# Optimization experiments

Measured on AMD Instinct MI355X. Metric: run time of the kernel, lower is better.

Reference implementation:

```python
import jax, jax.numpy as jnp
import numpy as np

N_WIRES = 12
N_QLAYERS = 2
DIM = 2 ** N_WIRES


def setup_inputs() -> dict:
    key = jax.random.key(0)
    k0, k1, k2, k3 = jax.random.split(key, 4)
    x = jax.random.normal(k0, (2048, 1024), dtype=jnp.float32)
    # TT cores: ranks [1,16,1], input dims [32,32], output dims [8,9]
    core0 = jax.random.normal(k1, (1, 32, 8, 16), dtype=jnp.float32) * 0.05
    core1 = jax.random.normal(k2, (16, 32, 9, 1), dtype=jnp.float32) * 0.05
    tt_bias = jnp.zeros((72,), dtype=jnp.float32)
    global_angles = jax.random.normal(k3, (N_QLAYERS, N_WIRES, 3), dtype=jnp.float32) * 0.1
    return {"x": x, "core0": core0, "core1": core1, "tt_bias": tt_bias,
            "global_angles": global_angles}


def _rot(angles):
    # angles [..., 3] -> combined U = Rz @ Ry @ Rx, shape [..., 2, 2] complex64
    half = angles * 0.5
    cx, sx = jnp.cos(half[..., 0]), jnp.sin(half[..., 0])
    cy, sy = jnp.cos(half[..., 1]), jnp.sin(half[..., 1])
    cz, sz = jnp.cos(half[..., 2]), jnp.sin(half[..., 2])
    zero = jnp.zeros_like(cx)
    cplx = jax.lax.complex
    Rx = jnp.stack([jnp.stack([cplx(cx, zero), cplx(zero, -sx)], -1),
                    jnp.stack([cplx(zero, -sx), cplx(cx, zero)], -1)], -2)
    Ry = jnp.stack([jnp.stack([cplx(cy, zero), cplx(-sy, zero)], -1),
                    jnp.stack([cplx(sy, zero), cplx(cy, zero)], -1)], -2)
    ez, ezc = cplx(cz, -sz), cplx(cz, sz)  # exp(-i z/2), exp(+i z/2)
    zc = cplx(zero, zero)
    Rz = jnp.stack([jnp.stack([ez, zc], -1), jnp.stack([zc, ezc], -1)], -2)
    return jnp.einsum('...ij,...jk,...kl->...il', Rz, Ry, Rx)


def _apply_1q(state, U, w):
    # state [bsz, 2^n]; U [bsz, 2, 2]; wire 0 = most significant qubit
    bsz = state.shape[0]
    left, right = 2 ** w, 2 ** (N_WIRES - w - 1)
    s = state.reshape(bsz, left, 2, right)
    s = jnp.einsum('bij,bljr->blir', U, s)
    return s.reshape(bsz, DIM)


def _cnot(state, c, t):
    bsz = state.shape[0]
    s = state.reshape((bsz,) + (2,) * N_WIRES)
    s0 = jax.lax.index_in_dim(s, 0, c + 1, keepdims=True)
    s1 = jax.lax.index_in_dim(s, 1, c + 1, keepdims=True)
    s1 = jnp.flip(s1, axis=t + 1)  # flip target amplitudes where control = 1
    return jnp.concatenate([s0, s1], axis=c + 1).reshape(bsz, DIM)


def reference(x, core0, core1, tt_bias, global_angles):
    bsz = x.shape[0]
    # --- TT layer: x[b,32,32] contracted with two TT cores -> [b,8,9] -> [b,72]
    x_rs = x.reshape(bsz, 32, 32)
    tt_out = jnp.einsum('bij,aipq,qjrs->bpr', x_rs, core0, core1).reshape(bsz, -1) + tt_bias
    # residual global angles
    angles = global_angles[None, :, :, :] + tt_out.reshape(bsz, N_QLAYERS, N_WIRES, 3)
    U = _rot(angles)  # [bsz, L, n, 2, 2]
    # --- tensor-product Ry encoding of x[:, :n_wires] on |0...0>
    enc = x[:, :N_WIRES] * 0.5
    amp = jnp.stack([jnp.cos(enc), jnp.sin(enc)], -1)  # [bsz, n, 2]
    state = amp[:, 0, :]
    for w in range(1, N_WIRES):
        state = (state[:, :, None] * amp[:, w, None, :]).reshape(bsz, -1)
    state = state.astype(jnp.complex64)  # [bsz, 2^n]
    # --- VQC layers: fused Rz@Ry@Rx per wire, then ring CNOT (noise_prob=0)
    for k in range(N_QLAYERS):
        for w in range(N_WIRES):
            state = _apply_1q(state, U[:, k, w], w)
        for i in range(N_WIRES - 1):
            state = _cnot(state, i, i + 1)
        state = _cnot(state, N_WIRES - 1, 0)
    # --- MeasureAll(PauliZ): <Z_w> per wire
    probs = jnp.real(state * jnp.conj(state))  # [bsz, 2^n]
    idx = jnp.arange(DIM)[:, None]
    bits = (idx >> jnp.arange(N_WIRES - 1, -1, -1)[None, :]) & 1  # [2^n, n]
    zsign = (1.0 - 2.0 * bits).astype(jnp.float32)
    return probs @ zsign  # [bsz, n_wires]
```

## Files before the change

kernel.cpp:

```cpp
#include <hip/hip_runtime.h>
#include <math.h>

#define N_WIRES 12

__host__ __device__ constexpr int parity12(int x) {
  x ^= x >> 8; x ^= x >> 4; x ^= x >> 2; x ^= x >> 1;
  return x & 1;
}

__global__ __launch_bounds__(256) void build_w_kernel(
    const float* __restrict__ core0,
    const float* __restrict__ core1,
    float* __restrict__ Wt) {
  int idx = blockIdx.x * 256 + threadIdx.x;
  int k = idx / 72;
  int o = idx - k * 72;
  int i = k >> 5, jj = k & 31;
  int p = o / 9, r = o - p * 9;
  float acc = 0.f;
#pragma unroll
  for (int q = 0; q < 16; ++q) {
    acc += core0[(i * 8 + p) * 16 + q] * core1[(q * 32 + jj) * 9 + r];
  }
  int og = o / 9, j = o - og * 9;
  Wt[k * 96 + og * 12 + j] = acc;
}

__global__ __launch_bounds__(512) void tt_gemm2(
    const float* __restrict__ x,
    const float* __restrict__ Wt,
    const float* __restrict__ bias,
    float* __restrict__ ttout) {
  __shared__ __align__(16) float ws[128 * 96];
  __shared__ __align__(16) float xs[8 * 132];
  __shared__ float part[16 * 8 * 73];
  const int t = threadIdx.x;
  const int row0 = blockIdx.x * 8;
  const int kk = t >> 5;
  const int rp = (t >> 3) & 3;
  const int og = t & 7;
  const int r0 = rp * 2;

  float a0[9], a1[9];
#pragma unroll
  for (int j = 0; j < 9; ++j) { a0[j] = 0.f; a1[j] = 0.f; }

  for (int s = 0; s < 8; ++s) {
    __syncthreads();
    const float4* Wg = (const float4*)(Wt + s * 128 * 96);
#pragma unroll
    for (int i = 0; i < 6; ++i) {
      const int idx = i * 512 + t;
      ((float4*)ws)[idx] = Wg[idx];
    }
    if (t < 256) {
      const int rr = t >> 5, j4 = t & 31;
      *(float4*)&xs[rr * 132 + j4 * 4] =
          *(const float4*)(x + (size_t)(row0 + rr) * 1024 + s * 128 + j4 * 4);
    }
    __syncthreads();
#pragma unroll
    for (int i = 0; i < 8; ++i) {
      const int k = kk + i * 16;
      const float4 wA = *(const float4*)&ws[k * 96 + og * 12];
      const float4 wB = *(const float4*)&ws[k * 96 + og * 12 + 4];
      const float w8 = ws[k * 96 + og * 12 + 8];
      const float x0v = xs[r0 * 132 + k];
      const float x1v = xs[r0 * 132 + 132 + k];
      a0[0] += x0v * wA.x; a0[1] += x0v * wA.y;
      a0[2] += x0v * wA.z; a0[3] += x0v * wA.w;
      a0[4] += x0v * wB.x; a0[5] += x0v * wB.y;
      a0[6] += x0v * wB.z; a0[7] += x0v * wB.w;
      a0[8] += x0v * w8;
      a1[0] += x1v * wA.x; a1[1] += x1v * wA.y;
      a1[2] += x1v * wA.z; a1[3] += x1v * wA.w;
      a1[4] += x1v * wB.x; a1[5] += x1v * wB.y;
      a1[6] += x1v * wB.z; a1[7] += x1v * wB.w;
      a1[8] += x1v * w8;
    }
  }

#pragma unroll
  for (int j = 0; j < 9; ++j) {
    part[(kk * 8 + r0) * 73 + og * 9 + j] = a0[j];
    part[(kk * 8 + r0 + 1) * 73 + og * 9 + j] = a1[j];
  }
  __syncthreads();

  for (int i = t; i < 576; i += 512) {
    const int r = i / 72, o = i - r * 72;
    float ssum = bias[o];
#pragma unroll
    for (int kq = 0; kq < 16; ++kq) ssum += part[(kq * 8 + r) * 73 + o];
    ttout[(size_t)(row0 + r) * 72 + o] = ssum;
  }
}

template <int MASK, int ROW>
__device__ __forceinline__ void apply_gate(
    float vr[16], float vi[16],
    float u00r, float u00i, float u01r, float u01i,
    float u10r, float u10i, float u11r, float u11i,
    float* __restrict__ buf, int t) {
  constexpr int RM = MASK & 15;
  constexpr int TM = (MASK >> 4) & 0xFF;
  constexpr int LM = TM & 63;
  constexpr bool LDSX = (TM & 0xC0) != 0;

  const int tpar = __popc(ROW & (t << 4)) & 1;
  const float aor = tpar ? u11r : u00r, aoi = tpar ? u11i : u00i;
  const float apr = tpar ? u10r : u01r, api = tpar ? u10i : u01i;
  const float qor = tpar ? u00r : u11r, qoi = tpar ? u00i : u11i;
  const float qpr = tpar ? u01r : u10r, qpi = tpar ? u01i : u10i;

  auto upd = [&](int r, float ar, float ai, float br, float bi,
                 float& xr, float& xi) {
    const bool b1 = parity12(ROW & r);
    const float cor = b1 ? qor : aor, coi = b1 ? qoi : aoi;
    const float cpr = b1 ? qpr : apr, cpi = b1 ? qpi : api;
    const float nr = cor * ar - coi * ai + cpr * br - cpi * bi;
    const float ni = cor * ai + coi * ar + cpr * bi + cpi * br;
    xr = nr; xi = ni;
  };

  if constexpr (LDSX) {
    const int tp = t ^ TM;
    if constexpr ((RM & 8) == 0) {
      __syncthreads();
#pragma unroll
      for (int r = 8; r < 16; ++r) {
        buf[(r & 7) * 256 + t] = vr[r];
        buf[2048 + (r & 7) * 256 + t] = vi[r];
      }
      __syncthreads();
#pragma unroll
      for (int r = 8; r < 16; ++r) {
        const int r2 = r ^ RM;
        const float br = buf[(r2 & 7) * 256 + tp];
        const float bi = buf[2048 + (r2 & 7) * 256 + tp];
        upd(r, vr[r], vi[r], br, bi, vr[r], vi[r]);
      }
      __syncthreads();
#pragma unroll
      for (int r = 0; r < 8; ++r) {
        buf[r * 256 + t] = vr[r];
        buf[2048 + r * 256 + t] = vi[r];
      }
      __syncthreads();
#pragma unroll
      for (int r = 0; r < 8; ++r) {
        const int r2 = r ^ RM;
        const float br = buf[r2 * 256 + tp];
        const float bi = buf[2048 + r2 * 256 + tp];
        upd(r, vr[r], vi[r], br, bi, vr[r], vi[r]);
      }
    } else {
      __syncthreads();
#pragma unroll
      for (int r = 8; r < 16; ++r) {
        buf[(r & 7) * 256 + t] = vr[r];
        buf[2048 + (r & 7) * 256 + t] = vi[r];
      }
      __syncthreads();
      float tr[8], ti[8];
#pragma unroll
      for (int r = 0; r < 8; ++r) {
        const int r2 = r ^ RM;
        const float br = buf[(r2 & 7) * 256 + tp];
        const float bi = buf[2048 + (r2 & 7) * 256 + tp];
        upd(r, vr[r], vi[r], br, bi, tr[r], ti[r]);
      }
      __syncthreads();
#pragma unroll
      for (int r = 0; r < 8; ++r) {
        buf[r * 256 + t] = vr[r];
        buf[2048 + r * 256 + t] = vi[r];
      }
      __syncthreads();
#pragma unroll
      for (int r = 8; r < 16; ++r) {
        const int r2 = r ^ RM;
        const float br = buf[r2 * 256 + tp];
        const float bi = buf[2048 + r2 * 256 + tp];
        upd(r, vr[r], vi[r], br, bi, vr[r], vi[r]);
      }
#pragma unroll
      for (int r = 0; r < 8; ++r) { vr[r] = tr[r]; vi[r] = ti[r]; }
    }
  } else if constexpr (LM != 0) {
    static_assert(!(LM != 0) || RM == 0, "shfl gates have no reg component");
#pragma unroll
    for (int r = 0; r < 16; ++r) {
      const float br = __shfl_xor(vr[r], LM, 64);
      const float bi = __shfl_xor(vi[r], LM, 64);
      upd(r, vr[r], vi[r], br, bi, vr[r], vi[r]);
    }
  } else {
#pragma unroll
    for (int r = 0; r < 16; ++r) {
      if (r < (r ^ RM)) {
        const int r2 = r ^ RM;
        const float ar = vr[r], ai = vi[r];
        const float br = vr[r2], bi = vi[r2];
        upd(r, ar, ai, br, bi, vr[r], vi[r]);
        upd(r2, br, bi, ar, ai, vr[r2], vi[r2]);
      }
    }
  }
}

__global__ __launch_bounds__(256, 5) void vqc_kernel3(
    const float* __restrict__ x,
    const float* __restrict__ ttout,
    const float* __restrict__ gang,
    float* __restrict__ out) {
  const int b = blockIdx.x;
  const int t = threadIdx.x;

  __shared__ __align__(16) float buf[4096];
  __shared__ float sUre[12][4], sUim[12][4];
  __shared__ float sFre[12][2], sFim[12][2];

  const float* ttb = ttout + (size_t)b * 72;

  if (t < 24) {
    const int w = (t < 12) ? t : t - 12;
    const int k = (t < 12) ? 1 : 0;
    const int gbase = (k * 12 + w) * 3;
    const int tbase = k * 36 + w * 3;
    float a0 = gang[gbase + 0] + ttb[tbase + 0];
    float a1 = gang[gbase + 1] + ttb[tbase + 1];
    float a2 = gang[gbase + 2] + ttb[tbase + 2];
    float cx = cosf(0.5f * a0), sx = sinf(0.5f * a0);
    float cy = cosf(0.5f * a1), sy = sinf(0.5f * a1);
    float cz = cosf(0.5f * a2), sz = sinf(0.5f * a2);
    float m00r = cy * cx,   m00i = sy * sx;
    float m01r = -sy * cx,  m01i = -cy * sx;
    float m10r = sy * cx,   m10i = -cy * sx;
    float m11r = cy * cx,   m11i = -sy * sx;
    float U00r = cz * m00r + sz * m00i, U00i = cz * m00i - sz * m00r;
    float U01r = cz * m01r + sz * m01i, U01i = cz * m01i - sz * m01r;
    float U10r = cz * m10r - sz * m10i, U10i = cz * m10i + sz * m10r;
    float U11r = cz * m11r - sz * m11i, U11i = cz * m11i + sz * m11r;
    if (t < 12) {
      sUre[w][0] = U00r; sUim[w][0] = U00i;
      sUre[w][1] = U01r; sUim[w][1] = U01i;
      sUre[w][2] = U10r; sUim[w][2] = U10i;
      sUre[w][3] = U11r; sUim[w][3] = U11i;
    } else {
      const float e = x[(size_t)b * 1024 + w] * 0.5f;
      const float c = cosf(e), s = sinf(e);
      sFre[w][0] = U00r * c + U01r * s;  sFim[w][0] = U00i * c + U01i * s;
      sFre[w][1] = U10r * c + U11r * s;  sFim[w][1] = U10i * c + U11i * s;
    }
  }
  __syncthreads();

  float vr[16], vi[16];
  {
    const int bits[7] = {(t >> 7) & 1,
                         ((t >> 6) ^ (t >> 5)) & 1,
                         ((t >> 5) ^ (t >> 4)) & 1,
                         ((t >> 4) ^ (t >> 3)) & 1,
                         ((t >> 3) ^ (t >> 2)) & 1,
                         ((t >> 2) ^ (t >> 1)) & 1,
                         ((t >> 1) ^ t) & 1};
    float br_ = 1.f, bi_ = 0.f;
#pragma unroll
    for (int w = 0; w < 7; ++w) {
      const float fr = sFre[w][bits[w]], fi = sFim[w][bits[w]];
      const float nr = br_ * fr - bi_ * fi;
      const float ni = br_ * fi + bi_ * fr;
      br_ = nr; bi_ = ni;
    }
    const int t0 = t & 1;
    float b7r[2], b7i[2];
#pragma unroll
    for (int r3 = 0; r3 < 2; ++r3) {
      const float fr = sFre[7][t0 ^ r3], fi = sFim[7][t0 ^ r3];
      b7r[r3] = br_ * fr - bi_ * fi;
      b7i[r3] = br_ * fi + bi_ * fr;
    }
    float hr[8], hi[8];
#pragma unroll
    for (int j = 0; j < 8; ++j) {
      const int r3 = j >> 2, r2 = (j >> 1) & 1, r1 = j & 1;
      const float ar = sFre[8][r3 ^ r2], ai = sFim[8][r3 ^ r2];
      const float cr = sFre[9][r2 ^ r1], ci = sFim[9][r2 ^ r1];
      hr[j] = ar * cr - ai * ci; hi[j] = ar * ci + ai * cr;
    }
    float gr[4], gi[4];
#pragma unroll
    for (int j = 0; j < 4; ++j) {
      const int r1 = j >> 1, r0 = j & 1;
      const float ar = sFre[10][r1 ^ r0], ai = sFim[10][r1 ^ r0];
      const float cr = sFre[11][r0], ci = sFim[11][r0];
      gr[j] = ar * cr - ai * ci; gi[j] = ar * ci + ai * cr;
    }
#pragma unroll
    for (int r = 0; r < 16; ++r) {
      const int r3 = r >> 3, hj = r >> 1, gj = r & 3;
      const float pr = hr[hj] * gr[gj] - hi[hj] * gi[gj];
      const float pi = hr[hj] * gi[gj] + hi[hj] * gr[gj];
      vr[r] = b7r[r3] * pr - b7i[r3] * pi;
      vi[r] = b7r[r3] * pi + b7i[r3] * pr;
    }
  }

#define GATE(MASK, ROW, GID)                                             \
  apply_gate<MASK, ROW>(vr, vi,                                          \
      sUre[GID][0], sUim[GID][0], sUre[GID][1], sUim[GID][1],            \
      sUre[GID][2], sUim[GID][2], sUre[GID][3], sUim[GID][3], buf, t)

  GATE(0xC00, 0x400, 0);
  GATE(0x200, 0xE00, 1);
  GATE(0x100, 0xD00, 2);
  GATE(0x080, 0xC80, 3);
  GATE(0x040, 0xC40, 4);
  GATE(0x020, 0xC20, 5);
  GATE(0x010, 0xC10, 6);
  GATE(0x008, 0xC08, 7);
  GATE(0x004, 0xC04, 8);
  GATE(0x002, 0xC02, 9);
  GATE(0x001, 0xC01, 10);
  GATE(0xBFF, 0xC00, 11);
#undef GATE

  constexpr int MROWS[12] = {0xFFF, 0xA00, 0x700, 0xB80, 0x7C0, 0xBE0,
                             0x7F0, 0xBF8, 0x7FC, 0xBFE, 0x7FF, 0xBFF};
  float acc[12];
#pragma unroll
  for (int w = 0; w < 12; ++w) acc[w] = 0.f;
#pragma unroll
  for (int r = 0; r < 16; ++r) {
    const float pr = vr[r] * vr[r] + vi[r] * vi[r];
#pragma unroll
    for (int w = 0; w < 12; ++w) {
      if (parity12(MROWS[w] & r)) acc[w] -= pr; else acc[w] += pr;
    }
  }
  __syncthreads();
#pragma unroll
  for (int w = 0; w < 12; ++w) {
    float v = (__popc(MROWS[w] & (t << 4)) & 1) ? -acc[w] : acc[w];
#pragma unroll
    for (int off = 32; off > 0; off >>= 1) v += __shfl_down(v, off, 64);
    if ((t & 63) == 0) buf[(t >> 6) * 12 + w] = v;
  }
  __syncthreads();
  if (t < 12) {
    out[(size_t)b * 12 + t] = buf[t] + buf[12 + t] + buf[24 + t] + buf[36 + t];
  }
}

extern "C" void kernel_launch(void* const* d_in, const int* in_sizes, int n_in,
                              void* d_out, int out_size, void* d_ws, size_t ws_size,
                              hipStream_t stream) {
  const float* x       = (const float*)d_in[0];
  const float* core0   = (const float*)d_in[1];
  const float* core1   = (const float*)d_in[2];
  const float* tt_bias = (const float*)d_in[3];
  const float* gang    = (const float*)d_in[4];
  float* out = (float*)d_out;
  float* Wt     = (float*)d_ws;
  float* ttout  = (float*)d_ws + 98304;

  const int bsz = in_sizes[0] / 1024;

  build_w_kernel<<<288, 256, 0, stream>>>(core0, core1, Wt);
  tt_gemm2<<<bsz / 8, 512, 0, stream>>>(x, Wt, tt_bias, ttout);
  vqc_kernel3<<<bsz, 256, 0, stream>>>(x, ttout, gang, out);
}
```

Before: 58.89 us.

## Pack statevector amplitudes into float2 pairs and use packed FMA gate updates

Reorganizes the per-thread statevector into float2 pairs of amplitudes whose gate coefficients are related by sign, so each gate update runs through v_pk_fma_f32/v_pk_mul_f32 inline asm. It exploits the SU(2) structure of the gate matrix (only u00 and u01 are needed) and turns the per-thread parity into sign-bit XORs. The LDS exchange is rewritten into two phases using float2 stores. The goal is to cut VALU instruction count in the gate-heavy loop, at the cost of swap moves, inline-asm register constraints, and more complex indexing.

After: 58.79 us. No clear change (-0.2%).

```diff
diff --git a/kernel.cpp b/kernel.cpp
--- a/kernel.cpp
+++ b/kernel.cpp
@@ -7,6 +7,19 @@
   x ^= x >> 8; x ^= x >> 4; x ^= x >> 2; x ^= x >> 1;
   return x & 1;
 }
+
+typedef float2 f2;
+__device__ __forceinline__ f2 mk2(float a, float b) { f2 r; r.x = a; r.y = b; return r; }
+__device__ __forceinline__ f2 pkmul(f2 a, f2 b) {
+  f2 d; asm("v_pk_mul_f32 %0, %1, %2" : "=v"(d) : "v"(a), "v"(b)); return d;
+}
+__device__ __forceinline__ f2 pkfma(f2 a, f2 b, f2 c) {
+  f2 d; asm("v_pk_fma_f32 %0, %1, %2, %3" : "=v"(d) : "v"(a), "v"(b), "v"(c)); return d;
+}
+__device__ __forceinline__ f2 shfl_xor2(f2 v, int m) {
+  f2 r; r.x = __shfl_xor(v.x, m, 64); r.y = __shfl_xor(v.y, m, 64); return r;
+}
+__device__ __forceinline__ f2 swap2(f2 v) { return mk2(v.y, v.x); }
 
 __global__ __launch_bounds__(256) void build_w_kernel(
     const float* __restrict__ core0,
@@ -97,119 +110,93 @@
 }
 
 template <int MASK, int ROW>
-__device__ __forceinline__ void apply_gate(
-    float vr[16], float vi[16],
+__device__ __forceinline__ void gate_pk(f2 R[8], f2 I[8],
     float u00r, float u00i, float u01r, float u01i,
-    float u10r, float u10i, float u11r, float u11i,
-    float* __restrict__ buf, int t) {
+    f2* __restrict__ buf, int t) {
   constexpr int RM = MASK & 15;
   constexpr int TM = (MASK >> 4) & 0xFF;
   constexpr int LM = TM & 63;
   constexpr bool LDSX = (TM & 0xC0) != 0;
-
-  const int tpar = __popc(ROW & (t << 4)) & 1;
-  const float aor = tpar ? u11r : u00r, aoi = tpar ? u11i : u00i;
-  const float apr = tpar ? u10r : u01r, api = tpar ? u10i : u01i;
-  const float qor = tpar ? u00r : u11r, qoi = tpar ? u00i : u11i;
-  const float qpr = tpar ? u01r : u10r, qpi = tpar ? u01i : u10i;
-
-  auto upd = [&](int r, float ar, float ai, float br, float bi,
-                 float& xr, float& xi) {
-    const bool b1 = parity12(ROW & r);
-    const float cor = b1 ? qor : aor, coi = b1 ? qoi : aoi;
-    const float cpr = b1 ? qpr : apr, cpi = b1 ? qpi : api;
-    const float nr = cor * ar - coi * ai + cpr * br - cpi * bi;
-    const float ni = cor * ai + coi * ar + cpr * bi + cpi * br;
-    xr = nr; xi = ni;
+  constexpr int FLIP = parity12(ROW & 3);
+  constexpr int JX = (RM == 0) ? 0 : (((RM & 1) ? (RM ^ 3) : RM) >> 1);
+  constexpr bool SW = (RM & 1) != 0;
+
+  const int tsgn = (__popc(ROW & (t << 4)) & 1) << 31;
+  const float dEi = __int_as_float(__float_as_int(u00i) ^ tsgn);
+  const float oEr = __int_as_float(__float_as_int(u01r) ^ tsgn);
+  const float ndEi = -dEi, noEr = -oEr;
+  const f2 A  = mk2(u00r, u00r);
+  const f2 C  = mk2(u01i, u01i);
+  const f2 nC = mk2(-u01i, -u01i);
+
+  auto Dof = [&](int pe, int ph) { return mk2(pe ? ndEi : dEi, ph ? ndEi : dEi); };
+  auto Oof = [&](int pe, int ph) { return mk2(pe ? noEr : oEr, ph ? noEr : oEr); };
+
+  auto upd = [&](int j, f2 Rb, f2 Ib, f2& outR, f2& outI) {
+    const int pe = parity12(ROW & (2 * j));
+    const int ph = pe ^ FLIP;
+    const f2 Dj = Dof(pe, ph), nDj = Dof(!pe, !ph), Oj = Oof(pe, ph);
+    const f2 a = R[j], ii = I[j];
+    outR = pkfma(A, a, pkfma(nDj, ii, pkfma(Oj, Rb, pkmul(nC, Ib))));
+    outI = pkfma(Dj, a, pkfma(A, ii, pkfma(C, Rb, pkmul(Oj, Ib))));
   };
 
   if constexpr (LDSX) {
     const int tp = t ^ TM;
-    if constexpr ((RM & 8) == 0) {
+#pragma unroll
+    for (int ph2 = 0; ph2 < 2; ++ph2) {
       __syncthreads();
 #pragma unroll
-      for (int r = 8; r < 16; ++r) {
-        buf[(r & 7) * 256 + t] = vr[r];
-        buf[2048 + (r & 7) * 256 + t] = vi[r];
+      for (int j = 0; j < 8; ++j) {
+        const bool inA = (j < 2) || (j > 5);
+        if ((ph2 == 0) == inA) {
+          const int slot = inA ? ((j < 2) ? j : j - 4) : (j - 2);
+          buf[slot * 512 + t] = R[j];
+          buf[slot * 512 + 256 + t] = I[j];
+        }
       }
       __syncthreads();
 #pragma unroll
-      for (int r = 8; r < 16; ++r) {
-        const int r2 = r ^ RM;
-        const float br = buf[(r2 & 7) * 256 + tp];
-        const float bi = buf[2048 + (r2 & 7) * 256 + tp];
-        upd(r, vr[r], vi[r], br, bi, vr[r], vi[r]);
+      for (int j = 0; j < 8; ++j) {
+        const bool inA = (j < 2) || (j > 5);
+        if ((ph2 == 0) == inA) {
+          const int j2 = j ^ JX;
+          const bool inA2 = (j2 < 2) || (j2 > 5);
+          const int slot2 = inA2 ? ((j2 < 2) ? j2 : j2 - 4) : (j2 - 2);
+          f2 Rb = buf[slot2 * 512 + tp];
+          f2 Ib = buf[slot2 * 512 + 256 + tp];
+          if constexpr (SW) { Rb = swap2(Rb); Ib = swap2(Ib); }
+          upd(j, Rb, Ib, R[j], I[j]);
+        }
       }
-      __syncthreads();
-#pragma unroll
-      for (int r = 0; r < 8; ++r) {
-        buf[r * 256 + t] = vr[r];
-        buf[2048 + r * 256 + t] = vi[r];
+    }
+  } else if constexpr (LM != 0) {
+#pragma unroll
+    for (int j = 0; j < 8; ++j) {
+      const f2 Rb = shfl_xor2(R[j], LM);
+      const f2 Ib = shfl_xor2(I[j], LM);
+      upd(j, Rb, Ib, R[j], I[j]);
+    }
+  } else {
+#pragma unroll
+    for (int j = 0; j < 8; ++j) {
+      const int j2 = j ^ JX;
+      if (j < j2) {
+        f2 Rb1 = R[j2], Ib1 = I[j2], Rb2 = R[j], Ib2 = I[j];
+        if constexpr (SW) {
+          Rb1 = swap2(Rb1); Ib1 = swap2(Ib1);
+          Rb2 = swap2(Rb2); Ib2 = swap2(Ib2);
+        }
+        f2 nR1, nI1, nR2, nI2;
+        upd(j, Rb1, Ib1, nR1, nI1);
+        upd(j2, Rb2, Ib2, nR2, nI2);
+        R[j] = nR1; I[j] = nI1; R[j2] = nR2; I[j2] = nI2;
       }
-      __syncthreads();
-#pragma unroll
-      for (int r = 0; r < 8; ++r) {
-        const int r2 = r ^ RM;
-        const float br = buf[r2 * 256 + tp];
-        const float bi = buf[2048 + r2 * 256 + tp];
-        upd(r, vr[r], vi[r], br, bi, vr[r], vi[r]);
-      }
-    } else {
-      __syncthreads();
-#pragma unroll
-      for (int r = 8; r < 16; ++r) {
-        buf[(r & 7) * 256 + t] = vr[r];
-        buf[2048 + (r & 7) * 256 + t] = vi[r];
-      }
-      __syncthreads();
-      float tr[8], ti[8];
-#pragma unroll
-      for (int r = 0; r < 8; ++r) {
-        const int r2 = r ^ RM;
-        const float br = buf[(r2 & 7) * 256 + tp];
-        const float bi = buf[2048 + (r2 & 7) * 256 + tp];
-        upd(r, vr[r], vi[r], br, bi, tr[r], ti[r]);
-      }
-      __syncthreads();
-#pragma unroll
-      for (int r = 0; r < 8; ++r) {
-        buf[r * 256 + t] = vr[r];
-        buf[2048 + r * 256 + t] = vi[r];
-      }
-      __syncthreads();
-#pragma unroll
-      for (int r = 8; r < 16; ++r) {
-        const int r2 = r ^ RM;
-        const float br = buf[r2 * 256 + tp];
-        const float bi = buf[2048 + r2 * 256 + tp];
-        upd(r, vr[r], vi[r], br, bi, vr[r], vi[r]);
-      }
-#pragma unroll
-      for (int r = 0; r < 8; ++r) { vr[r] = tr[r]; vi[r] = ti[r]; }
-    }
-  } else if constexpr (LM != 0) {
-    static_assert(!(LM != 0) || RM == 0, "shfl gates have no reg component");
-#pragma unroll
-    for (int r = 0; r < 16; ++r) {
-      const float br = __shfl_xor(vr[r], LM, 64);
-      const float bi = __shfl_xor(vi[r], LM, 64);
-      upd(r, vr[r], vi[r], br, bi, vr[r], vi[r]);
-    }
-  } else {
-#pragma unroll
-    for (int r = 0; r < 16; ++r) {
-      if (r < (r ^ RM)) {
-        const int r2 = r ^ RM;
-        const float ar = vr[r], ai = vi[r];
-        const float br = vr[r2], bi = vi[r2];
-        upd(r, ar, ai, br, bi, vr[r], vi[r]);
-        upd(r2, br, bi, ar, ai, vr[r2], vi[r2]);
-      }
-    }
-  }
-}
-
-__global__ __launch_bounds__(256, 5) void vqc_kernel3(
+    }
+  }
+}
+
+__global__ __launch_bounds__(256, 5) void vqc_kernel4(
     const float* __restrict__ x,
     const float* __restrict__ ttout,
     const float* __restrict__ gang,
@@ -217,8 +204,8 @@
   const int b = blockIdx.x;
   const int t = threadIdx.x;
 
-  __shared__ __align__(16) float buf[4096];
-  __shared__ float sUre[12][4], sUim[12][4];
+  __shared__ __align__(16) f2 buf[2048];
+  __shared__ float sU[12][4];
   __shared__ float sFre[12][2], sFim[12][2];
 
   const float* ttb = ttout + (size_t)b * 72;
@@ -243,10 +230,8 @@
     float U10r = cz * m10r - sz * m10i, U10i = cz * m10i + sz * m10r;
     float U11r = cz * m11r - sz * m11i, U11i = cz * m11i + sz * m11r;
     if (t < 12) {
-      sUre[w][0] = U00r; sUim[w][0] = U00i;
-      sUre[w][1] = U01r; sUim[w][1] = U01i;
-      sUre[w][2] = U10r; sUim[w][2] = U10i;
-      sUre[w][3] = U11r; sUim[w][3] = U11i;
+      sU[w][0] = U00r; sU[w][1] = U00i;
+      sU[w][2] = U01r; sU[w][3] = U01i;
     } else {
       const float e = x[(size_t)b * 1024 + w] * 0.5f;
       const float c = cosf(e), s = sinf(e);
@@ -306,11 +291,15 @@
       vi[r] = b7r[r3] * pi + b7i[r3] * pr;
     }
   }
-
-#define GATE(MASK, ROW, GID)                                             \
-  apply_gate<MASK, ROW>(vr, vi,                                          \
-      sUre[GID][0], sUim[GID][0], sUre[GID][1], sUim[GID][1],            \
-      sUre[GID][2], sUim[GID][2], sUre[GID][3], sUim[GID][3], buf, t)
+  f2 R[8], I[8];
+#pragma unroll
+  for (int j = 0; j < 8; ++j) {
+    R[j] = mk2(vr[2 * j], vr[(2 * j) ^ 3]);
+    I[j] = mk2(vi[2 * j], vi[(2 * j) ^ 3]);
+  }
+
+#define GATE(MASK, ROW, GID) \
+  gate_pk<MASK, ROW>(R, I, sU[GID][0], sU[GID][1], sU[GID][2], sU[GID][3], buf, t)
 
   GATE(0xC00, 0x400, 0);
   GATE(0x200, 0xE00, 1);
@@ -328,28 +317,35 @@
 
   constexpr int MROWS[12] = {0xFFF, 0xA00, 0x700, 0xB80, 0x7C0, 0xBE0,
                              0x7F0, 0xBF8, 0x7FC, 0xBFE, 0x7FF, 0xBFF};
-  float acc[12];
-#pragma unroll
-  for (int w = 0; w < 12; ++w) acc[w] = 0.f;
-#pragma unroll
-  for (int r = 0; r < 16; ++r) {
-    const float pr = vr[r] * vr[r] + vi[r] * vi[r];
+  const f2 Spp = mk2(1.f, 1.f),  Smm = mk2(-1.f, -1.f);
+  const f2 Spm = mk2(1.f, -1.f), Smp = mk2(-1.f, 1.f);
+  f2 acc2[12];
+#pragma unroll
+  for (int w = 0; w < 12; ++w) acc2[w] = mk2(0.f, 0.f);
+#pragma unroll
+  for (int j = 0; j < 8; ++j) {
+    const f2 pr2 = pkfma(I[j], I[j], pkmul(R[j], R[j]));
 #pragma unroll
     for (int w = 0; w < 12; ++w) {
-      if (parity12(MROWS[w] & r)) acc[w] -= pr; else acc[w] += pr;
+      const int sl = parity12(MROWS[w] & (2 * j));
+      const int sh = sl ^ parity12(MROWS[w] & 3);
+      const f2 S = sl ? (sh ? Smm : Smp) : (sh ? Spm : Spp);
+      acc2[w] = pkfma(S, pr2, acc2[w]);
     }
   }
   __syncthreads();
+  float* rbuf = (float*)buf;
 #pragma unroll
   for (int w = 0; w < 12; ++w) {
-    float v = (__popc(MROWS[w] & (t << 4)) & 1) ? -acc[w] : acc[w];
+    float v = acc2[w].x + acc2[w].y;
+    if (__popc(MROWS[w] & (t << 4)) & 1) v = -v;
 #pragma unroll
     for (int off = 32; off > 0; off >>= 1) v += __shfl_down(v, off, 64);
-    if ((t & 63) == 0) buf[(t >> 6) * 12 + w] = v;
+    if ((t & 63) == 0) rbuf[(t >> 6) * 12 + w] = v;
   }
   __syncthreads();
   if (t < 12) {
-    out[(size_t)b * 12 + t] = buf[t] + buf[12 + t] + buf[24 + t] + buf[36 + t];
+    out[(size_t)b * 12 + t] = rbuf[t] + rbuf[12 + t] + rbuf[24 + t] + rbuf[36 + t];
   }
 }
 
@@ -369,5 +365,5 @@
 
   build_w_kernel<<<288, 256, 0, stream>>>(core0, core1, Wt);
   tt_gemm2<<<bsz / 8, 512, 0, stream>>>(x, Wt, tt_bias, ttout);
-  vqc_kernel3<<<bsz, 256, 0, stream>>>(x, ttout, gang, out);
-}
+  vqc_kernel4<<<bsz, 256, 0, stream>>>(x, ttout, gang, out);
+}
```
